# Kernel tuning notes

Measured on AMD Instinct MI355X. Metric: run time of the kernel, lower is better.

Reference implementation:

```python
import jax, jax.numpy as jnp
import numpy as np

N_NODES = 8192
N_EDGES = 262144  # avg degree 32
F_IN = 128
F_OUT = 128


def setup_inputs() -> dict:
    key = jax.random.key(0)
    k1, k2, k3, k4 = jax.random.split(key, 4)
    x = jax.random.normal(k1, (N_NODES, F_IN), dtype=jnp.float32)
    edge_index = jax.random.randint(k2, (2, N_EDGES), 0, N_NODES, dtype=jnp.int32)
    # xavier_uniform-scale random W; B is a learned param (zeros at init, but
    # use random values so the x@B^T branch is exercised numerically)
    scale = np.float32(1.0 / np.sqrt(F_IN))
    W = jax.random.normal(k3, (F_OUT, F_IN), dtype=jnp.float32) * scale
    B = jax.random.normal(k4, (F_OUT, F_IN), dtype=jnp.float32) * scale
    return {"x": x, "edge_index": edge_index, "W": W, "B": B}


def reference(x, edge_index, W, B):
    num_nodes = x.shape[0]
    src, dst = edge_index[0], edge_index[1]
    # Dense adjacency: A[i, j] = 1 iff edge j -> i (duplicate edges collapse to 1,
    # matching torch's adj[dst, src] = 1.0 assignment semantics)
    A = jnp.zeros((num_nodes, num_nodes), dtype=jnp.float32).at[dst, src].set(1.0)
    # In-degree (counts duplicate edges, matching torch.bincount); degree-0 -> 1
    deg = jax.ops.segment_sum(jnp.ones_like(dst, dtype=jnp.float32), dst,
                              num_segments=num_nodes)
    deg = jnp.where(deg == 0, 1.0, deg)
    # D_inv @ A @ x @ W^T + x @ B^T; D_inv is diagonal -> row-scale by 1/deg
    msg = A @ (x @ W.T)           # [N, F_OUT]
    out = msg / deg[:, None] + x @ B.T
    return out
```

## Files before the change

### kernel.cpp

```cpp
#include <hip/hip_runtime.h>
#include <hip/hip_bf16.h>

constexpr int NN = 8192;
constexpr int NE = 262144;
constexpr int FD = 128;
constexpr int NG = 8;
constexpr unsigned int CAPG = 32;

constexpr size_t H_OFF     = 0;
constexpr size_t H_BYTES   = (size_t)NN * FD * 2;
constexpr size_t CNT_OFF   = H_OFF + H_BYTES;
constexpr size_t CNT_BYTES = (size_t)NG * NN * 4;
constexpr size_t COL_OFF   = CNT_OFF + CNT_BYTES;
constexpr size_t COL_BYTES = (size_t)NN * NG * CAPG * 4;
constexpr size_t UB_OFF    = COL_OFF + COL_BYTES;

constexpr int FILL_BLOCKS = 512;
constexpr int GEMM_BLOCKS = 512;

typedef __attribute__((ext_vector_type(8))) short short8;
typedef __attribute__((ext_vector_type(4))) float f32x4;

__device__ __forceinline__ short f2b(float f) {
  union { __hip_bfloat16 b; short s; } u;
  u.b = __float2bfloat16(f);
  return u.s;
}

__device__ __forceinline__ short8 cvt8(float4 a, float4 b) {
  return short8{f2b(a.x), f2b(a.y), f2b(a.z), f2b(a.w),
                f2b(b.x), f2b(b.y), f2b(b.z), f2b(b.w)};
}

__global__ __launch_bounds__(256) void prep_kernel(
    const float* __restrict__ W, const float* __restrict__ Bm,
    short* __restrict__ ub, unsigned int* __restrict__ cnt8) {
  const int t = blockIdx.x * 256 + threadIdx.x;
  if (t < 8192) {
    const float4 f = (t < 4096) ? ((const float4*)W)[t]
                                : ((const float4*)Bm)[t - 4096];
    ((short4*)ub)[t] = short4{f2b(f.x), f2b(f.y), f2b(f.z), f2b(f.w)};
  }
  ((uint4*)cnt8)[t] = uint4{0u, 0u, 0u, 0u};
}

__global__ __launch_bounds__(256) void fillgemm_kernel(
    const int* __restrict__ ei, unsigned int* __restrict__ cnt8,
    int* __restrict__ col, const float* __restrict__ x,
    const short* __restrict__ ub, __hip_bfloat16* __restrict__ h,
    float* __restrict__ out) {
  const int tid = threadIdx.x;

  if (blockIdx.x < FILL_BLOCKS) {
    const int g = blockIdx.x & (NG - 1);
    const int e = (blockIdx.x * 256 + tid) * 2;
    const int2 s2 = *(const int2*)(ei + e);
    const int2 d2 = *(const int2*)(ei + NE + e);
#pragma unroll
    for (int r = 0; r < 2; ++r) {
      const int src = (&s2.x)[r];
      const int dst = (&d2.x)[r];
      const unsigned int pos = atomicAdd(&cnt8[(size_t)g * NN + dst], 1u);
      if (pos < CAPG) col[((size_t)dst * NG + g) * CAPG + pos] = src;
    }
    return;
  }

  const int gid = blockIdx.x - FILL_BLOCKS;
  const int bm = (gid >> 2) * 64;
  const int bn = (gid & 3) * 64;
  const int w = tid >> 6;
  const int lane = tid & 63;
  const int l15 = lane & 15;
  const int l4 = lane >> 4;
  const int row0 = bm + w * 16;

  f32x4 acc[4] = {};

#pragma unroll
  for (int kk = 0; kk < 4; ++kk) {
    const int koff = kk * 32 + l4 * 8;
    const float4* xp = (const float4*)(x + (size_t)(row0 + l15) * FD + koff);
    const short8 a = cvt8(xp[0], xp[1]);
#pragma unroll
    for (int ni = 0; ni < 4; ++ni) {
      const short8 b = *(const short8*)(ub + (size_t)(bn + ni * 16 + l15) * FD + koff);
      acc[ni] = __builtin_amdgcn_mfma_f32_16x16x32_bf16(a, b, acc[ni], 0, 0, 0);
    }
  }

#pragma unroll
  for (int ni = 0; ni < 4; ++ni) {
    const int n = bn + ni * 16 + l15;
#pragma unroll
    for (int r = 0; r < 4; ++r) {
      const int row = row0 + l4 * 4 + r;
      const float v = acc[ni][r];
      if (n < FD) h[(size_t)row * FD + n] = __float2bfloat16(v);
      else        out[(size_t)row * FD + (n - FD)] = v;
    }
  }
}

__global__ __launch_bounds__(256) void gather_kernel(
    const unsigned int* __restrict__ h,
    const int* __restrict__ col, const unsigned int* __restrict__ cnt8,
    float* __restrict__ out) {
  __shared__ unsigned int bmp[4][NN / 32];
  __shared__ int list[4][64];

  const int w    = threadIdx.x >> 6;
  const int lane = threadIdx.x & 63;
  const int node = blockIdx.x * 4 + w;
  const int c  = lane & 15;
  const int eu = lane >> 4;

  unsigned int cg = 0;
  if (lane < NG) cg = cnt8[(size_t)lane * NN + node];

  ((uint4*)bmp[w])[lane] = uint4{0u, 0u, 0u, 0u};
  list[w][lane] = -1;
  __syncthreads();

  unsigned int n_deg = 0, abase = 0;
#pragma unroll
  for (int g = 0; g < NG; ++g) {
    const unsigned int v = __shfl(cg, g, 64);
    const unsigned int vc = (v < CAPG) ? v : CAPG;
    const unsigned int idx = abase + lane;
    if (lane < (int)vc && idx < 64u)
      list[w][idx] = col[((size_t)node * NG + g) * CAPG + lane];
    n_deg += v;
    abase += vc;
  }
  const unsigned int nn = (abase < 64u) ? abase : 64u;
  __syncthreads();

  if (lane < (int)nn) {
    const int s = list[w][lane];
    if (s >= 0) {
      const unsigned int mask = 1u << (s & 31);
      const unsigned int old = atomicOr(&bmp[w][s >> 5], mask);
      if (old & mask) list[w][lane] = -1;
    }
  }
  __syncthreads();

  float acc[8];
#pragma unroll
  for (int i = 0; i < 8; ++i) acc[i] = 0.f;

  const size_t hstride = FD / 2;

  for (unsigned int base = 0; base < nn; base += 8) {
    const int s0 = list[w][base + eu];
    const int s1 = list[w][base + 4 + eu];
    uint4 v0 = uint4{0u,0u,0u,0u}, v1 = uint4{0u,0u,0u,0u};
    if (s0 >= 0) v0 = *(const uint4*)(h + (size_t)s0 * hstride + (c << 2));
    if (s1 >= 0) v1 = *(const uint4*)(h + (size_t)s1 * hstride + (c << 2));
    acc[0] += __uint_as_float(v0.x << 16) + __uint_as_float(v1.x << 16);
    acc[1] += __uint_as_float(v0.x & 0xffff0000u) + __uint_as_float(v1.x & 0xffff0000u);
    acc[2] += __uint_as_float(v0.y << 16) + __uint_as_float(v1.y << 16);
    acc[3] += __uint_as_float(v0.y & 0xffff0000u) + __uint_as_float(v1.y & 0xffff0000u);
    acc[4] += __uint_as_float(v0.z << 16) + __uint_as_float(v1.z << 16);
    acc[5] += __uint_as_float(v0.z & 0xffff0000u) + __uint_as_float(v1.z & 0xffff0000u);
    acc[6] += __uint_as_float(v0.w << 16) + __uint_as_float(v1.w << 16);
    acc[7] += __uint_as_float(v0.w & 0xffff0000u) + __uint_as_float(v1.w & 0xffff0000u);
  }

#pragma unroll
  for (int i = 0; i < 8; ++i) {
    acc[i] += __shfl_xor(acc[i], 16, 64);
    acc[i] += __shfl_xor(acc[i], 32, 64);
  }

  if (eu == 0) {
    const float r = 1.0f / (n_deg ? (float)n_deg : 1.0f);
    float* op = out + (size_t)node * FD + c * 8;
    float4 o0 = *(float4*)op;
    float4 o1 = *(float4*)(op + 4);
    o0.x += acc[0] * r; o0.y += acc[1] * r; o0.z += acc[2] * r; o0.w += acc[3] * r;
    o1.x += acc[4] * r; o1.y += acc[5] * r; o1.z += acc[6] * r; o1.w += acc[7] * r;
    *(float4*)op = o0;
    *(float4*)(op + 4) = o1;
  }
}

extern "C" void kernel_launch(void* const* d_in, const int* in_sizes, int n_in,
                              void* d_out, int out_size, void* d_ws, size_t ws_size,
                              hipStream_t stream) {
  const float* x  = (const float*)d_in[0];
  const int* ei   = (const int*)d_in[1];
  const float* W  = (const float*)d_in[2];
  const float* Bm = (const float*)d_in[3];
  float* out = (float*)d_out;

  char* ws = (char*)d_ws;
  __hip_bfloat16* h  = (__hip_bfloat16*)(ws + H_OFF);
  unsigned int* cnt8 = (unsigned int*)(ws + CNT_OFF);
  int* col           = (int*)(ws + COL_OFF);
  short* ub          = (short*)(ws + UB_OFF);

  prep_kernel<<<64, 256, 0, stream>>>(W, Bm, ub, cnt8);
  fillgemm_kernel<<<FILL_BLOCKS + GEMM_BLOCKS, 256, 0, stream>>>(
      ei, cnt8, col, x, ub, h, out);
  gather_kernel<<<NN / 4, 256, 0, stream>>>((const unsigned int*)h, col, cnt8, out);
}
```

Baseline: 39.06 us.

## Bucket edges by destination slice with shared-memory counters instead of global atomics

The edge-fill phase now has 256 blocks, each owning a slice of 256 destination nodes and a segment of the edge list. Each block scans its segment's dst array, counts matching edges with LDS atomics and scatters src into per-node, per-segment buckets, then writes the counts once. This removes the global atomicAdd contention of the old scheme. In exchange every block reads 1/8 of the edge list while keeping only about 1/32 of it, so dst data is read redundantly. The gather list grows to 96 entries with a second dedup pass, and with a per-segment cap of 24 and a total cap of 96, unusually high in-degree nodes could lose edges.

```diff
diff --git a/kernel.cpp b/kernel.cpp
--- a/kernel.cpp
+++ b/kernel.cpp
@@ -4,18 +4,23 @@
 constexpr int NN = 8192;
 constexpr int NE = 262144;
 constexpr int FD = 128;
-constexpr int NG = 8;
-constexpr unsigned int CAPG = 32;
+
+constexpr int NSLICE = 32;
+constexpr int NSEG   = 8;
+constexpr int SLICE_N = NN / NSLICE;
+constexpr int SEG_E   = NE / NSEG;
+constexpr int CAPJ    = 24;
+constexpr int LCAP    = 96;
 
 constexpr size_t H_OFF     = 0;
 constexpr size_t H_BYTES   = (size_t)NN * FD * 2;
 constexpr size_t CNT_OFF   = H_OFF + H_BYTES;
-constexpr size_t CNT_BYTES = (size_t)NG * NN * 4;
+constexpr size_t CNT_BYTES = (size_t)NN * NSEG * 4;
 constexpr size_t COL_OFF   = CNT_OFF + CNT_BYTES;
-constexpr size_t COL_BYTES = (size_t)NN * NG * CAPG * 4;
+constexpr size_t COL_BYTES = (size_t)NN * NSEG * CAPJ * 4;
 constexpr size_t UB_OFF    = COL_OFF + COL_BYTES;
 
-constexpr int FILL_BLOCKS = 512;
+constexpr int FILL_BLOCKS = NSLICE * NSEG;
 constexpr int GEMM_BLOCKS = 512;
 
 typedef __attribute__((ext_vector_type(8))) short short8;
@@ -34,35 +39,54 @@
 
 __global__ __launch_bounds__(256) void prep_kernel(
     const float* __restrict__ W, const float* __restrict__ Bm,
-    short* __restrict__ ub, unsigned int* __restrict__ cnt8) {
+    short* __restrict__ ub, unsigned int* __restrict__ cnt) {
   const int t = blockIdx.x * 256 + threadIdx.x;
+  ((uint4*)cnt)[t] = uint4{0u, 0u, 0u, 0u};
   if (t < 8192) {
     const float4 f = (t < 4096) ? ((const float4*)W)[t]
                                 : ((const float4*)Bm)[t - 4096];
     ((short4*)ub)[t] = short4{f2b(f.x), f2b(f.y), f2b(f.z), f2b(f.w)};
   }
-  ((uint4*)cnt8)[t] = uint4{0u, 0u, 0u, 0u};
 }
 
 __global__ __launch_bounds__(256) void fillgemm_kernel(
-    const int* __restrict__ ei, unsigned int* __restrict__ cnt8,
+    const int* __restrict__ ei, unsigned int* __restrict__ cnt,
     int* __restrict__ col, const float* __restrict__ x,
     const short* __restrict__ ub, __hip_bfloat16* __restrict__ h,
     float* __restrict__ out) {
   const int tid = threadIdx.x;
 
   if (blockIdx.x < FILL_BLOCKS) {
-    const int g = blockIdx.x & (NG - 1);
-    const int e = (blockIdx.x * 256 + tid) * 2;
-    const int2 s2 = *(const int2*)(ei + e);
-    const int2 d2 = *(const int2*)(ei + NE + e);
-#pragma unroll
-    for (int r = 0; r < 2; ++r) {
-      const int src = (&s2.x)[r];
-      const int dst = (&d2.x)[r];
-      const unsigned int pos = atomicAdd(&cnt8[(size_t)g * NN + dst], 1u);
-      if (pos < CAPG) col[((size_t)dst * NG + g) * CAPG + pos] = src;
-    }
+    __shared__ unsigned int lcnt[SLICE_N];
+    const int slice = blockIdx.x >> 3;
+    const int seg   = blockIdx.x & 7;
+    const int nlo   = slice * SLICE_N;
+    const int ebase = seg * SEG_E;
+
+    lcnt[tid] = 0u;
+    __syncthreads();
+
+    const int4* dst4 = (const int4*)(ei + NE + ebase);
+#pragma unroll 4
+    for (int it = 0; it < SEG_E / (256 * 4); ++it) {
+      const int idx = it * 256 + tid;
+      const int4 d4 = dst4[idx];
+#pragma unroll
+      for (int r = 0; r < 4; ++r) {
+        const int dst = (&d4.x)[r];
+        const int loc = dst - nlo;
+        if ((unsigned)loc < (unsigned)SLICE_N) {
+          const unsigned int pos = atomicAdd(&lcnt[loc], 1u);
+          if (pos < CAPJ) {
+            const int src = ei[ebase + idx * 4 + r];
+            col[((size_t)dst * NSEG + seg) * CAPJ + pos] = src;
+          }
+        }
+      }
+    }
+    __syncthreads();
+
+    cnt[(size_t)(nlo + tid) * NSEG + seg] = lcnt[tid];
     return;
   }
 
@@ -104,10 +128,10 @@
 
 __global__ __launch_bounds__(256) void gather_kernel(
     const unsigned int* __restrict__ h,
-    const int* __restrict__ col, const unsigned int* __restrict__ cnt8,
+    const int* __restrict__ col, const unsigned int* __restrict__ cnt,
     float* __restrict__ out) {
   __shared__ unsigned int bmp[4][NN / 32];
-  __shared__ int list[4][64];
+  __shared__ int list[4][LCAP];
 
   const int w    = threadIdx.x >> 6;
   const int lane = threadIdx.x & 63;
@@ -116,24 +140,26 @@
   const int eu = lane >> 4;
 
   unsigned int cg = 0;
-  if (lane < NG) cg = cnt8[(size_t)lane * NN + node];
+  if (lane < NSEG) cg = cnt[(size_t)node * NSEG + lane];
 
   ((uint4*)bmp[w])[lane] = uint4{0u, 0u, 0u, 0u};
   list[w][lane] = -1;
+  if (lane < LCAP - 64) list[w][64 + lane] = -1;
   __syncthreads();
 
   unsigned int n_deg = 0, abase = 0;
-#pragma unroll
-  for (int g = 0; g < NG; ++g) {
+  const int* cbase = col + (size_t)node * NSEG * CAPJ;
+#pragma unroll
+  for (int g = 0; g < NSEG; ++g) {
     const unsigned int v = __shfl(cg, g, 64);
-    const unsigned int vc = (v < CAPG) ? v : CAPG;
+    const unsigned int vc = (v < (unsigned)CAPJ) ? v : (unsigned)CAPJ;
     const unsigned int idx = abase + lane;
-    if (lane < (int)vc && idx < 64u)
-      list[w][idx] = col[((size_t)node * NG + g) * CAPG + lane];
+    if (lane < (int)vc && idx < (unsigned)LCAP)
+      list[w][idx] = cbase[g * CAPJ + lane];
     n_deg += v;
     abase += vc;
   }
-  const unsigned int nn = (abase < 64u) ? abase : 64u;
+  const unsigned int nn = (abase < (unsigned)LCAP) ? abase : (unsigned)LCAP;
   __syncthreads();
 
   if (lane < (int)nn) {
@@ -142,6 +168,14 @@
       const unsigned int mask = 1u << (s & 31);
       const unsigned int old = atomicOr(&bmp[w][s >> 5], mask);
       if (old & mask) list[w][lane] = -1;
+    }
+  }
+  if (lane + 64 < (int)nn) {
+    const int s = list[w][lane + 64];
+    if (s >= 0) {
+      const unsigned int mask = 1u << (s & 31);
+      const unsigned int old = atomicOr(&bmp[w][s >> 5], mask);
+      if (old & mask) list[w][lane + 64] = -1;
     }
   }
   __syncthreads();
@@ -196,13 +230,13 @@
   float* out = (float*)d_out;
 
   char* ws = (char*)d_ws;
-  __hip_bfloat16* h  = (__hip_bfloat16*)(ws + H_OFF);
-  unsigned int* cnt8 = (unsigned int*)(ws + CNT_OFF);
-  int* col           = (int*)(ws + COL_OFF);
-  short* ub          = (short*)(ws + UB_OFF);
-
-  prep_kernel<<<64, 256, 0, stream>>>(W, Bm, ub, cnt8);
+  __hip_bfloat16* h = (__hip_bfloat16*)(ws + H_OFF);
+  unsigned int* cnt = (unsigned int*)(ws + CNT_OFF);
+  int* col          = (int*)(ws + COL_OFF);
+  short* ub         = (short*)(ws + UB_OFF);
+
+  prep_kernel<<<64, 256, 0, stream>>>(W, Bm, ub, cnt);
   fillgemm_kernel<<<FILL_BLOCKS + GEMM_BLOCKS, 256, 0, stream>>>(
-      ei, cnt8, col, x, ub, h, out);
-  gather_kernel<<<NN / 4, 256, 0, stream>>>((const unsigned int*)h, col, cnt8, out);
-}
+      ei, cnt, col, x, ub, h, out);
+  gather_kernel<<<NN / 4, 256, 0, stream>>>((const unsigned int*)h, col, cnt, out);
+}
```

Measured after the change: 53.95 us. 38.1% more time.
